# Performance work log

Measured on AMD Instinct MI355X. Metric: run time of the kernel, lower is better.

## Reference

```python
import math
import jax, jax.numpy as jnp
import numpy as np

HIDDEN = 1024
NUM_HEADS = 16
NUM_QUERIES = 2
NUM_Q_HEADS = NUM_HEADS * NUM_QUERIES  # 32
HEAD_DIM = 64
Q_DIM = NUM_Q_HEADS * HEAD_DIM   # 2048
KV_DIM = NUM_HEADS * HEAD_DIM    # 1024
BATCH, SEQ = 4, 1024


def _alibi_slopes(num_heads: int) -> np.ndarray:
    # num_heads is a power of two here, so only the main branch applies
    closest_pow2 = 2 ** int(math.floor(math.log2(num_heads)))
    base = 2.0 ** (-(2.0 ** (-(math.log2(closest_pow2) - 3))))
    powers = np.arange(1, closest_pow2 + 1, dtype=np.float32)
    slopes = base ** powers
    if closest_pow2 != num_heads:
        extra_base = 2.0 ** (-(2.0 ** (-(math.log2(2 * closest_pow2) - 3))))
        extra_powers = np.arange(1, 2 * (num_heads - closest_pow2) + 1, 2, dtype=np.float32)
        slopes = np.concatenate([slopes, extra_base ** extra_powers])
    return slopes[:num_heads].astype(np.float32)

ALIBI_SLOPES = jnp.asarray(_alibi_slopes(NUM_Q_HEADS))  # (32,)


def setup_inputs() -> dict:
    key = jax.random.key(0)
    k1, k2, k3 = jax.random.split(key, 3)
    inputs = jax.random.normal(k1, (BATCH, SEQ, HIDDEN), dtype=jnp.float32)
    # match nn.Linear default init scale roughly
    W_qkv = jax.random.normal(k2, (HIDDEN, Q_DIM + 2 * KV_DIM), dtype=jnp.float32) * (1.0 / math.sqrt(HIDDEN))
    W_out = jax.random.normal(k3, (Q_DIM, HIDDEN), dtype=jnp.float32) * (1.0 / math.sqrt(Q_DIM))
    return {"inputs": inputs, "W_qkv": W_qkv, "W_out": W_out}


def reference(inputs, W_qkv, W_out):
    B, S, _ = inputs.shape
    qkv = inputs @ W_qkv                                   # [B,S,4096]
    q = qkv[..., :Q_DIM].reshape(B, S, NUM_Q_HEADS, HEAD_DIM).transpose(0, 2, 1, 3)   # [B,32,S,64]
    k = qkv[..., Q_DIM:Q_DIM + KV_DIM].reshape(B, S, NUM_HEADS, HEAD_DIM).transpose(0, 2, 1, 3)
    v = qkv[..., Q_DIM + KV_DIM:].reshape(B, S, NUM_HEADS, HEAD_DIM).transpose(0, 2, 1, 3)
    # GQA: repeat_interleave along head dim
    k = jnp.repeat(k, NUM_QUERIES, axis=1)                 # [B,32,S,64]
    v = jnp.repeat(v, NUM_QUERIES, axis=1)
    # ALiBi bias: slope_h * (kv_pos - q_pos)
    pos = jnp.arange(S)
    rel = (pos[None, :] - pos[:, None]).astype(jnp.float32)           # [S,S]
    bias = ALIBI_SLOPES[:, None, None] * rel[None, :, :]              # [32,S,S]
    scores = jnp.einsum('bhqd,bhkd->bhqk', q, k) / math.sqrt(HEAD_DIM)
    scores = scores + bias[None]
    causal = pos[:, None] >= pos[None, :]                             # [S,S]
    scores = jnp.where(causal[None, None], scores, -jnp.inf)
    attn = jax.nn.softmax(scores, axis=-1)
    out = jnp.einsum('bhqk,bhkd->bhqd', attn, v)                      # [B,32,S,64]
    out = out.transpose(0, 2, 1, 3).reshape(B, S, Q_DIM)
    return out @ W_out                                                # [B,S,HIDDEN]
```

## Files before the change

### kernel.cpp

```cpp
#include <hip/hip_runtime.h>

typedef unsigned short u16;
typedef unsigned int u32;
typedef float f32x4 __attribute__((ext_vector_type(4)));
typedef float f32x16 __attribute__((ext_vector_type(16)));
typedef __bf16 bf16x8 __attribute__((ext_vector_type(8)));
typedef short short8 __attribute__((ext_vector_type(8)));
typedef u16 u16x4 __attribute__((ext_vector_type(4)));
typedef float f32x4v __attribute__((ext_vector_type(4)));

#define DEV __device__ __forceinline__

DEV u16 f2bf(float f) {
    union { float f; unsigned u; } v; v.f = f;
    unsigned r = v.u + 0x7FFFu + ((v.u >> 16) & 1u);
    return (u16)(r >> 16);
}

DEV void gload_lds16(const u16* g, u16* l) {
    __builtin_amdgcn_global_load_lds(
        (const __attribute__((address_space(1))) void*)g,
        (__attribute__((address_space(3))) void*)l, 16, 0, 0);
}

__global__ __launch_bounds__(256) void k_cvt(const float* __restrict__ in,
                                             u16* __restrict__ out, int n4) {
    int i = blockIdx.x * 256 + threadIdx.x;
    if (i >= n4) return;
    f32x4v v = reinterpret_cast<const f32x4v*>(in)[i];
    u16x4 o;
    o.x = f2bf(v.x); o.y = f2bf(v.y); o.z = f2bf(v.z); o.w = f2bf(v.w);
    reinterpret_cast<u16x4*>(out)[i] = o;
}

__global__ __launch_bounds__(256) void k_transpose_cvt(const float* __restrict__ in,
                                                       u16* __restrict__ out,
                                                       int R, int C) {
    __shared__ float tile[32][33];
    const int c0 = blockIdx.x * 32, r0 = blockIdx.y * 32;
    const int tx = threadIdx.x & 31, ty = threadIdx.x >> 5;
#pragma unroll
    for (int i = 0; i < 32; i += 8)
        tile[ty + i][tx] = in[(size_t)(r0 + ty + i) * C + c0 + tx];
    __syncthreads();
#pragma unroll
    for (int i = 0; i < 32; i += 8)
        out[(size_t)(c0 + ty + i) * R + r0 + tx] = f2bf(tile[tx][ty + i]);
}

template <int OUTF>
__global__ __launch_bounds__(256) void k_gemm_nt(const u16* __restrict__ A,
                                                 const u16* __restrict__ Bt,
                                                 void* __restrict__ Cv,
                                                 int M, int N, int K) {
    __shared__ u16 lA[2][4096];
    __shared__ u16 lB[2][4096];
    const int t = threadIdx.x, l = t & 63, w = t >> 6;
    const int bm = blockIdx.y * 128, bn = blockIdx.x * 128;
    const int wr = w >> 1, wc = w & 1;
    const int lm = l & 15, lg = l >> 4;

    f32x4 acc[4][4] = {};

    const int nk = K >> 5;
    auto stage = [&](int buf, int kt) {
        const int k0 = kt << 5;
        const int kc = (l & 3) * 8;
        const int rsub = w * 16 + (l >> 2);
#pragma unroll
        for (int p = 0; p < 2; ++p) {
            const int row = p * 64 + rsub;
            gload_lds16(A + (size_t)(bm + row) * K + k0 + kc, &lA[buf][p * 2048 + w * 512]);
            gload_lds16(Bt + (size_t)(bn + row) * K + k0 + kc, &lB[buf][p * 2048 + w * 512]);
        }
    };

    stage(0, 0);
    __syncthreads();
    for (int kt = 0; kt < nk; ++kt) {
        const int buf = kt & 1;
        if (kt + 1 < nk) stage(buf ^ 1, kt + 1);
        bf16x8 af[4], bfr[4];
#pragma unroll
        for (int i = 0; i < 4; ++i) {
            af[i]  = *reinterpret_cast<const bf16x8*>(&lA[buf][(wr * 64 + i * 16 + lm) * 32 + lg * 8]);
            bfr[i] = *reinterpret_cast<const bf16x8*>(&lB[buf][(wc * 64 + i * 16 + lm) * 32 + lg * 8]);
        }
        __builtin_amdgcn_s_setprio(1);
#pragma unroll
        for (int mi = 0; mi < 4; ++mi)
#pragma unroll
            for (int ni = 0; ni < 4; ++ni)
                acc[mi][ni] = __builtin_amdgcn_mfma_f32_16x16x32_bf16(af[mi], bfr[ni], acc[mi][ni], 0, 0, 0);
        __builtin_amdgcn_s_setprio(0);
        __syncthreads();
    }

#pragma unroll
    for (int mi = 0; mi < 4; ++mi)
#pragma unroll
        for (int ni = 0; ni < 4; ++ni)
#pragma unroll
            for (int r = 0; r < 4; ++r) {
                const int row = bm + wr * 64 + mi * 16 + lg * 4 + r;
                const int col = bn + wc * 64 + ni * 16 + lm;
                if (OUTF)
                    reinterpret_cast<float*>(Cv)[(size_t)row * N + col] = acc[mi][ni][r];
                else
                    reinterpret_cast<u16*>(Cv)[(size_t)row * N + col] = f2bf(acc[mi][ni][r]);
            }
}

__global__ __launch_bounds__(512, 4) void k_attn(const u16* __restrict__ qkv,
                                                 u16* __restrict__ AO) {
    __shared__ u16 lK[4096];
    __shared__ u16 lVT[4096];
    __shared__ float lSc[8][32];

    const int t = threadIdx.x, l = t & 63, w = t >> 6;
    const int lo5 = l & 31, hi = l >> 5;
    const int qb = blockIdx.x;
    const int hq = blockIdx.y;
    const int b  = blockIdx.z;
    const int hkv = hq >> 1;
    const float L2E = 1.44269504088896f;
    const float slope2 = exp2f(-0.25f * (float)(hq + 1)) * L2E;
    const float scale2 = 0.125f * L2E;
    const size_t RS = 4096;
    const u16* Qg = qkv + (size_t)(b * 1024 + qb * 256) * RS + hq * 64;
    const u16* Kg = qkv + (size_t)(b * 1024) * RS + 2048 + hkv * 64;
    const u16* Vg = qkv + (size_t)(b * 1024) * RS + 3072 + hkv * 64;

    const int q = qb * 256 + w * 32 + lo5;

    bf16x8 qfr[4];
#pragma unroll
    for (int ks = 0; ks < 4; ++ks)
        qfr[ks] = *reinterpret_cast<const bf16x8*>(
            Qg + (size_t)(w * 32 + lo5) * RS + ks * 16 + hi * 8);

    f32x16 acc0 = {}, acc1 = {};
    float m_ = -3.0e38f, l_ = 0.f;

    const int nt = (qb + 1) * 4;
    const int kbd = (qb * 256 + w * 32 + 31) >> 6;

    for (int kb = 0; kb < nt; ++kb) {
        {
            const int row = t >> 3;
            const int ch = (t & 7) ^ (row & 7);
            gload_lds16(Kg + (size_t)(kb * 64 + row) * RS + ch * 8, &lK[w * 512]);
        }
        {
            const int kv = t >> 3, d0 = (t & 7) * 8;
            short8 v = *reinterpret_cast<const short8*>(Vg + (size_t)(kb * 64 + kv) * RS + d0);
            const int kvs = (kv & ~12) | ((kv & 4) << 1) | ((kv & 8) >> 1);
#pragma unroll
            for (int j = 0; j < 8; ++j) {
                const int d = d0 + j;
                const int key = (d ^ (d >> 3)) & 7;
                lVT[d * 64 + (((kvs >> 3) ^ key) & 7) * 8 + (kvs & 7)] = (u16)v[j];
            }
        }
        __syncthreads();

        if (kb <= kbd) {
            f32x16 sc0 = {}, sc1 = {};
#pragma unroll
            for (int ks = 0; ks < 4; ++ks) {
                const int csw = ((ks * 2 + hi) ^ (lo5 & 7)) * 8;
                bf16x8 ka0 = *reinterpret_cast<const bf16x8*>(&lK[lo5 * 64 + csw]);
                bf16x8 ka1 = *reinterpret_cast<const bf16x8*>(&lK[(32 + lo5) * 64 + csw]);
                __builtin_amdgcn_s_setprio(1);
                sc0 = __builtin_amdgcn_mfma_f32_32x32x16_bf16(ka0, qfr[ks], sc0, 0, 0, 0);
                sc1 = __builtin_amdgcn_mfma_f32_32x32x16_bf16(ka1, qfr[ks], sc1, 0, 0, 0);
                __builtin_amdgcn_s_setprio(0);
            }
            float s[32];
            const float b0 = slope2 * (float)(kb * 64 + 4 * hi - q);
            const float b1 = slope2 * (float)(kb * 64 + 32 + 4 * hi - q);
#pragma unroll
            for (int r = 0; r < 16; ++r) {
                const int Cr = (r & 3) + 8 * (r >> 2);
                s[r]      = fmaf(sc0[r], scale2, fmaf(slope2, (float)Cr, b0));
                s[16 + r] = fmaf(sc1[r], scale2, fmaf(slope2, (float)Cr, b1));
            }
            if (kb == kbd) {
                const int qr0 = q - kb * 64 - 4 * hi;
#pragma unroll
                for (int r = 0; r < 16; ++r) {
                    const int Cr = (r & 3) + 8 * (r >> 2);
                    if (Cr > qr0)      s[r]      = -3.0e38f;
                    if (Cr + 32 > qr0) s[16 + r] = -3.0e38f;
                }
            }
            float tm[16];
#pragma unroll
            for (int i = 0; i < 16; ++i) tm[i] = fmaxf(s[i], s[16 + i]);
#pragma unroll
            for (int i = 0; i < 8; ++i) tm[i] = fmaxf(tm[i], tm[8 + i]);
#pragma unroll
            for (int i = 0; i < 4; ++i) tm[i] = fmaxf(tm[i], tm[4 + i]);
            float mx = fmaxf(fmaxf(tm[0], tm[1]), fmaxf(tm[2], tm[3]));
            mx = fmaxf(mx, __shfl_xor(mx, 32));
            const float mnew = fmaxf(m_, mx);
            const float sclf = exp2f(m_ - mnew);
            m_ = mnew;
#pragma unroll
            for (int i = 0; i < 32; ++i) s[i] = exp2f(s[i] - mnew);
            float ts[16];
#pragma unroll
            for (int i = 0; i < 16; ++i) ts[i] = s[i] + s[16 + i];
#pragma unroll
            for (int i = 0; i < 8; ++i) ts[i] += ts[8 + i];
#pragma unroll
            for (int i = 0; i < 4; ++i) ts[i] += ts[4 + i];
            float sum = (ts[0] + ts[1]) + (ts[2] + ts[3]);
            sum += __shfl_xor(sum, 32);
            l_ = l_ * sclf + sum;
            lSc[w][lo5] = sclf;
            asm volatile("s_waitcnt lgkmcnt(0)" ::: "memory");
            float rs_[16];
#pragma unroll
            for (int r = 0; r < 16; ++r) {
                const int Cr = (r & 3) + 8 * (r >> 2);
                rs_[r] = lSc[w][Cr + 4 * hi];
            }
#pragma unroll
            for (int r = 0; r < 16; ++r) { acc0[r] *= rs_[r]; acc1[r] *= rs_[r]; }
            u32 pw[16];
#pragma unroll
            for (int s4 = 0; s4 < 4; ++s4) {
                const int off = (s4 >> 1) * 16 + (s4 & 1) * 8;
#pragma unroll
                for (int j = 0; j < 4; ++j) {
                    u32 o;
                    asm("v_cvt_pk_bf16_f32 %0, %1, %2"
                        : "=v"(o) : "v"(s[off + 2 * j]), "v"(s[off + 2 * j + 1]));
                    pw[s4 * 4 + j] = o;
                }
            }
            const int key0 = (lo5 ^ (lo5 >> 3)) & 7;
            const int key1 = ((32 + lo5) ^ ((32 + lo5) >> 3)) & 7;
#pragma unroll
            for (int s4 = 0; s4 < 4; ++s4) {
                bf16x8 pa;
                u32* paw = reinterpret_cast<u32*>(&pa);
                paw[0] = pw[s4 * 4 + 0]; paw[1] = pw[s4 * 4 + 1];
                paw[2] = pw[s4 * 4 + 2]; paw[3] = pw[s4 * 4 + 3];
                const int cl = s4 * 2 + hi;
                bf16x8 va0 = *reinterpret_cast<const bf16x8*>(&lVT[lo5 * 64 + ((cl ^ key0) & 7) * 8]);
                bf16x8 va1 = *reinterpret_cast<const bf16x8*>(&lVT[(32 + lo5) * 64 + ((cl ^ key1) & 7) * 8]);
                __builtin_amdgcn_s_setprio(1);
                acc0 = __builtin_amdgcn_mfma_f32_32x32x16_bf16(pa, va0, acc0, 0, 0, 0);
                acc1 = __builtin_amdgcn_mfma_f32_32x32x16_bf16(pa, va1, acc1, 0, 0, 0);
                __builtin_amdgcn_s_setprio(0);
            }
        }
        __syncthreads();
    }

    lSc[w][lo5] = 1.0f / l_;
    asm volatile("s_waitcnt lgkmcnt(0)" ::: "memory");
    float rl[16];
#pragma unroll
    for (int r = 0; r < 16; ++r) {
        const int Cr = (r & 3) + 8 * (r >> 2);
        rl[r] = lSc[w][Cr + 4 * hi];
    }
    u16* AOp = AO + (size_t)(b * 1024 + qb * 256 + w * 32) * 2048 + hq * 64;
#pragma unroll
    for (int r = 0; r < 16; ++r) {
        const int Cr = (r & 3) + 8 * (r >> 2);
        const size_t rowoff = (size_t)(Cr + 4 * hi) * 2048;
        AOp[rowoff + lo5]      = f2bf(acc0[r] * rl[r]);
        AOp[rowoff + 32 + lo5] = f2bf(acc1[r] * rl[r]);
    }
}

extern "C" void kernel_launch(void* const* d_in, const int* in_sizes, int n_in,
                              void* d_out, int out_size, void* d_ws, size_t ws_size,
                              hipStream_t stream) {
    const float* X    = (const float*)d_in[0];
    const float* Wqkv = (const float*)d_in[1];
    const float* Wout = (const float*)d_in[2];
    float* out = (float*)d_out;

    char* ws = (char*)d_ws;
    u16* Xb    = (u16*)(ws);
    u16* WqkvT = (u16*)(ws + (size_t)(8  << 20));
    u16* WoutT = (u16*)(ws + (size_t)(16 << 20));
    u16* QKV   = (u16*)(ws + (size_t)(20 << 20));
    u16* AO    = (u16*)(ws + (size_t)(52 << 20));

    k_cvt<<<4096, 256, 0, stream>>>(X, Xb, (4096 * 1024) / 4);
    k_transpose_cvt<<<dim3(128, 32), 256, 0, stream>>>(Wqkv, WqkvT, 1024, 4096);
    k_transpose_cvt<<<dim3(32, 64), 256, 0, stream>>>(Wout, WoutT, 2048, 1024);

    k_gemm_nt<0><<<dim3(32, 32), 256, 0, stream>>>(Xb, WqkvT, QKV, 4096, 4096, 1024);

    k_attn<<<dim3(4, 32, 4), 512, 0, stream>>>(QKV, AO);

    k_gemm_nt<1><<<dim3(8, 32), 256, 0, stream>>>(AO, WoutT, out, 4096, 1024, 2048);
}
```

Before: 284.6 us.

## Double-buffer K/V tiles in attention and reorder blocks for causal load balance

The attention kernel now double-buffers K and transposed V in LDS and prefetches the next tile while the current one is computed. This removes one barrier per iteration and hides global load latency. V is now loaded by half the threads as row pairs and written to LDS with packed 32-bit stores. The grid is flattened so that heavy causal query blocks (qb=3) are dispatched first and paired with light ones, to balance the work across CUs. The cost is twice the LDS per block, which may reduce occupancy, and more live registers for the prefetched V.

```diff
diff --git a/kernel.cpp b/kernel.cpp
--- a/kernel.cpp
+++ b/kernel.cpp
@@ -113,15 +113,17 @@
 
 __global__ __launch_bounds__(512, 4) void k_attn(const u16* __restrict__ qkv,
                                                  u16* __restrict__ AO) {
-    __shared__ u16 lK[4096];
-    __shared__ u16 lVT[4096];
+    __shared__ u16 lK[2][4096];
+    __shared__ u16 lVT[2][4096];
     __shared__ float lSc[8][32];
 
     const int t = threadIdx.x, l = t & 63, w = t >> 6;
     const int lo5 = l & 31, hi = l >> 5;
-    const int qb = blockIdx.x;
-    const int hq = blockIdx.y;
-    const int b  = blockIdx.z;
+    const int fid = blockIdx.x;
+    const int half = fid >> 8, idx = fid & 255;
+    const int j = idx & 1, hb = idx >> 1;
+    const int hq = hb >> 2, b = hb & 3;
+    const int qb = half ? (j ? 2 : 0) : (j ? 1 : 3);
     const int hkv = hq >> 1;
     const float L2E = 1.44269504088896f;
     const float slope2 = exp2f(-0.25f * (float)(hq + 1)) * L2E;
@@ -145,32 +147,49 @@
     const int nt = (qb + 1) * 4;
     const int kbd = (qb * 256 + w * 32 + 31) >> 6;
 
+    auto stageK = [&](int buf, int kb) {
+        const int row = t >> 3;
+        const int ch = (t & 7) ^ (row & 7);
+        gload_lds16(Kg + (size_t)(kb * 64 + row) * RS + ch * 8, &lK[buf][w * 512]);
+    };
+    const int kvp = t >> 3, vd0 = (t & 7) * 8;
+    auto loadV = [&](int kb, short8& a, short8& b2) {
+        a  = *reinterpret_cast<const short8*>(Vg + (size_t)(kb * 64 + kvp * 2) * RS + vd0);
+        b2 = *reinterpret_cast<const short8*>(Vg + (size_t)(kb * 64 + kvp * 2 + 1) * RS + vd0);
+    };
+    auto writeV = [&](int buf, short8 a, short8 b2) {
+        const int kv0 = kvp * 2;
+        const int kvs0 = (kv0 & ~12) | ((kv0 & 4) << 1) | ((kv0 & 8) >> 1);
+#pragma unroll
+        for (int jj = 0; jj < 8; ++jj) {
+            const int d = vd0 + jj;
+            const int key = (d ^ (d >> 3)) & 7;
+            const u32 val = (u32)(u16)a[jj] | ((u32)(u16)b2[jj] << 16);
+            *reinterpret_cast<u32*>(
+                &lVT[buf][d * 64 + (((kvs0 >> 3) ^ key) & 7) * 8 + (kvs0 & 7)]) = val;
+        }
+    };
+
+    short8 vA, vB;
+    stageK(0, 0);
+    if (t < 256) { loadV(0, vA, vB); writeV(0, vA, vB); }
+    __syncthreads();
+
     for (int kb = 0; kb < nt; ++kb) {
-        {
-            const int row = t >> 3;
-            const int ch = (t & 7) ^ (row & 7);
-            gload_lds16(Kg + (size_t)(kb * 64 + row) * RS + ch * 8, &lK[w * 512]);
-        }
-        {
-            const int kv = t >> 3, d0 = (t & 7) * 8;
-            short8 v = *reinterpret_cast<const short8*>(Vg + (size_t)(kb * 64 + kv) * RS + d0);
-            const int kvs = (kv & ~12) | ((kv & 4) << 1) | ((kv & 8) >> 1);
-#pragma unroll
-            for (int j = 0; j < 8; ++j) {
-                const int d = d0 + j;
-                const int key = (d ^ (d >> 3)) & 7;
-                lVT[d * 64 + (((kvs >> 3) ^ key) & 7) * 8 + (kvs & 7)] = (u16)v[j];
-            }
-        }
-        __syncthreads();
+        const int buf = kb & 1;
+        const bool pre = (kb + 1 < nt);
+        if (pre) {
+            stageK(buf ^ 1, kb + 1);
+            if (t < 256) loadV(kb + 1, vA, vB);
+        }
 
         if (kb <= kbd) {
             f32x16 sc0 = {}, sc1 = {};
 #pragma unroll
             for (int ks = 0; ks < 4; ++ks) {
                 const int csw = ((ks * 2 + hi) ^ (lo5 & 7)) * 8;
-                bf16x8 ka0 = *reinterpret_cast<const bf16x8*>(&lK[lo5 * 64 + csw]);
-                bf16x8 ka1 = *reinterpret_cast<const bf16x8*>(&lK[(32 + lo5) * 64 + csw]);
+                bf16x8 ka0 = *reinterpret_cast<const bf16x8*>(&lK[buf][lo5 * 64 + csw]);
+                bf16x8 ka1 = *reinterpret_cast<const bf16x8*>(&lK[buf][(32 + lo5) * 64 + csw]);
                 __builtin_amdgcn_s_setprio(1);
                 sc0 = __builtin_amdgcn_mfma_f32_32x32x16_bf16(ka0, qfr[ks], sc0, 0, 0, 0);
                 sc1 = __builtin_amdgcn_mfma_f32_32x32x16_bf16(ka1, qfr[ks], sc1, 0, 0, 0);
@@ -233,11 +252,11 @@
             for (int s4 = 0; s4 < 4; ++s4) {
                 const int off = (s4 >> 1) * 16 + (s4 & 1) * 8;
 #pragma unroll
-                for (int j = 0; j < 4; ++j) {
+                for (int jj = 0; jj < 4; ++jj) {
                     u32 o;
                     asm("v_cvt_pk_bf16_f32 %0, %1, %2"
-                        : "=v"(o) : "v"(s[off + 2 * j]), "v"(s[off + 2 * j + 1]));
-                    pw[s4 * 4 + j] = o;
+                        : "=v"(o) : "v"(s[off + 2 * jj]), "v"(s[off + 2 * jj + 1]));
+                    pw[s4 * 4 + jj] = o;
                 }
             }
             const int key0 = (lo5 ^ (lo5 >> 3)) & 7;
@@ -249,14 +268,16 @@
                 paw[0] = pw[s4 * 4 + 0]; paw[1] = pw[s4 * 4 + 1];
                 paw[2] = pw[s4 * 4 + 2]; paw[3] = pw[s4 * 4 + 3];
                 const int cl = s4 * 2 + hi;
-                bf16x8 va0 = *reinterpret_cast<const bf16x8*>(&lVT[lo5 * 64 + ((cl ^ key0) & 7) * 8]);
-                bf16x8 va1 = *reinterpret_cast<const bf16x8*>(&lVT[(32 + lo5) * 64 + ((cl ^ key1) & 7) * 8]);
+                bf16x8 va0 = *reinterpret_cast<const bf16x8*>(&lVT[buf][lo5 * 64 + ((cl ^ key0) & 7) * 8]);
+                bf16x8 va1 = *reinterpret_cast<const bf16x8*>(&lVT[buf][(32 + lo5) * 64 + ((cl ^ key1) & 7) * 8]);
                 __builtin_amdgcn_s_setprio(1);
                 acc0 = __builtin_amdgcn_mfma_f32_32x32x16_bf16(pa, va0, acc0, 0, 0, 0);
                 acc1 = __builtin_amdgcn_mfma_f32_32x32x16_bf16(pa, va1, acc1, 0, 0, 0);
                 __builtin_amdgcn_s_setprio(0);
             }
         }
+
+        if (pre && t < 256) writeV(buf ^ 1, vA, vB);
         __syncthreads();
     }
 
@@ -299,7 +320,7 @@
 
     k_gemm_nt<0><<<dim3(32, 32), 256, 0, stream>>>(Xb, WqkvT, QKV, 4096, 4096, 1024);
 
-    k_attn<<<dim3(4, 32, 4), 512, 0, stream>>>(QKV, AO);
+    k_attn<<<dim3(512), 512, 0, stream>>>(QKV, AO);
 
     k_gemm_nt<1><<<dim3(8, 32), 256, 0, stream>>>(AO, WoutT, out, 4096, 1024, 2048);
 }
```

Result: faster. 264.5 us (-7.1%).
